# Performance work log

Measured on AMD Instinct MI355X. Metric: run time of the kernel, lower is better.

## Reference

```python
import jax, jax.numpy as jnp
import numpy as np

NUM_HEADS = 8

def setup_inputs() -> dict:
    key = jax.random.key(0)
    ks = jax.random.split(key, 7)
    B, Cin, H, W = 4, 256, 56, 56
    Cout = 256
    s = 1.0 / np.sqrt(Cin)
    return {
        "x": jax.random.normal(ks[0], (B, Cin, H, W), dtype=jnp.float32),
        "wq": jax.random.normal(ks[1], (Cout, Cin), dtype=jnp.float32) * s,
        "bq": jax.random.normal(ks[2], (Cout,), dtype=jnp.float32) * s,
        "wk": jax.random.normal(ks[3], (Cout, Cin), dtype=jnp.float32) * s,
        "bk": jax.random.normal(ks[4], (Cout,), dtype=jnp.float32) * s,
        "wv": jax.random.normal(ks[5], (Cout, Cin), dtype=jnp.float32) * s,
        "bv": jax.random.normal(ks[6], (Cout,), dtype=jnp.float32) * s,
    }

def _proj(x, w, b):
    # 1x1 conv == per-pixel linear: [B,Cin,H,W] x [Cout,Cin] -> [B,Cout,H,W]
    return jnp.einsum('bchw,oc->bohw', x, w) + b[None, :, None, None]

def reference(x, wq, bq, wk, bk, wv, bv):
    B, _, H, W = x.shape
    Cout = wq.shape[0]
    hd = Cout // NUM_HEADS
    N = H * W
    # project and reshape to [B, heads, N, head_dim]
    def split_heads(t):
        return t.reshape(B, NUM_HEADS, hd, N).transpose(0, 1, 3, 2)
    q = split_heads(_proj(x, wq, bq))
    k = split_heads(_proj(x, wk, bk))
    v = split_heads(_proj(x, wv, bv))
    scores = jnp.einsum('bhnd,bhmd->bhnm', q, k) / jnp.sqrt(jnp.float32(hd))
    attn = jax.nn.softmax(scores, axis=-1)          # [B, heads, N, N]
    out = jnp.einsum('bhnm,bhmd->bhnd', attn, v)    # [B, heads, N, hd]
    out = out.transpose(0, 1, 3, 2).reshape(B, Cout, H, W)
    return out
```

## Files before the change

### kernel.cpp

```cpp
#include <hip/hip_runtime.h>
#include <math.h>


#define NB   4
#define CIN  256
#define NPIX 3136
#define NH   8
#define HD   32
#define QSC  0.25503837897544295f

typedef float          f32x4  __attribute__((ext_vector_type(4)));
typedef short          bf16x8 __attribute__((ext_vector_type(8)));
typedef unsigned int   u32x4  __attribute__((ext_vector_type(4)));
typedef unsigned int   u32x2  __attribute__((ext_vector_type(2)));
typedef unsigned short u16x4  __attribute__((ext_vector_type(4)));

static __device__ __forceinline__ unsigned short f2bf(float f) {
  union { float f; unsigned u; } v; v.f = f;
  return (unsigned short)((v.u + 0x7fffu + ((v.u >> 16) & 1u)) >> 16);
}

static __device__ __forceinline__ float fast_exp2(float x) {
  float r;
  asm("v_exp_f32 %0, %1" : "=v"(r) : "v"(x));
  return r;
}

static __device__ __forceinline__ unsigned cvt_pk_bf16(float lo, float hi) {
  unsigned r;
  asm("v_cvt_pk_bf16_f32 %0, %1, %2" : "=v"(r) : "v"(lo), "v"(hi));
  return r;
}

static __device__ __forceinline__ void gload_lds16(const void* g, void* l) {
  __builtin_amdgcn_global_load_lds(
      (__attribute__((address_space(1))) const void*)g,
      (__attribute__((address_space(3))) void*)l, 16, 0, 0);
}

static __device__ __forceinline__ bf16x8 lds_frag16(const unsigned char* p) {
  u32x4 u = *(const u32x4*)p;
  return __builtin_bit_cast(bf16x8, u);
}

__global__ __launch_bounds__(256) void k_xpose(const float* __restrict__ x,
                                               unsigned short* __restrict__ xbT) {
  __shared__ unsigned short tile[64][66];
  const int n0 = blockIdx.x * 64, c0 = blockIdx.y * 64, b = blockIdx.z;
  const int t = threadIdx.x;
  const int cl = t >> 4, nl = (t & 15) * 4;
#pragma unroll
  for (int rep = 0; rep < 4; ++rep) {
    const int c = cl + rep * 16;
    f32x4 v = *(const f32x4*)(x + ((size_t)(b * CIN + c0 + c)) * NPIX + n0 + nl);
    tile[nl + 0][c] = f2bf(v.x);
    tile[nl + 1][c] = f2bf(v.y);
    tile[nl + 2][c] = f2bf(v.z);
    tile[nl + 3][c] = f2bf(v.w);
  }
  __syncthreads();
  const int nr = t >> 2, co = (t & 3) * 16;
  unsigned pw[8];
#pragma unroll
  for (int j = 0; j < 8; ++j)
    pw[j] = (unsigned)tile[nr][co + 2 * j] | ((unsigned)tile[nr][co + 2 * j + 1] << 16);
  unsigned short* dst = xbT + ((size_t)(b * NPIX + n0 + nr)) * 256 + c0 + co;
  u32x4 lo = {pw[0], pw[1], pw[2], pw[3]};
  u32x4 hi = {pw[4], pw[5], pw[6], pw[7]};
  *(u32x4*)dst = lo;
  *(u32x4*)(dst + 8) = hi;
}

__global__ __launch_bounds__(256) void k_wconv(const float* __restrict__ wq,
                                               const float* __restrict__ wk,
                                               const float* __restrict__ wv,
                                               unsigned short* __restrict__ wb) {
  const int i = blockIdx.x * 256 + threadIdx.x;
  const int mat = i >> 16, idx = i & 65535;
  const float* w = (mat == 0) ? wq : (mat == 1 ? wk : wv);
  const float s = (mat == 0) ? QSC : 1.0f;
  wb[i] = f2bf(w[idx] * s);
}

__global__ __launch_bounds__(256) void k_proj(
    const unsigned short* __restrict__ xbT, const unsigned short* __restrict__ wb,
    const float* __restrict__ bq, const float* __restrict__ bk,
    const float* __restrict__ bv,
    unsigned short* __restrict__ qws, unsigned short* __restrict__ kws,
    unsigned short* __restrict__ vtws) {
  __shared__ alignas(16) unsigned char lds[20480];
  const int b = blockIdx.y & 3, mat = blockIdx.y >> 2;
  const int n0 = blockIdx.x * 64;
  const int t = threadIdx.x, l = t & 63, wid = t >> 6, g = l >> 4, q = l & 15;
  const unsigned short* wmat = wb + mat * (256 * 256);

  f32x4 acc[4][4] = {};

  for (int ks = 0; ks < 8; ++ks) {
#pragma unroll
    for (int r = 0; r < 4; ++r) {
      const unsigned short* src = wmat + ((wid + 4 * r) * 16 + q) * 256 + ks * 32 + g * 8;
      gload_lds16(src, lds + (r * 256 + t) * 16);
    }
    gload_lds16(xbT + ((size_t)(b * NPIX + n0 + wid * 16 + q)) * 256 + ks * 32 + g * 8,
                lds + 16384 + t * 16);
    __syncthreads();

    bf16x8 wa[4], xf[4];
#pragma unroll
    for (int r = 0; r < 4; ++r) wa[r] = lds_frag16(lds + (r * 256 + wid * 64 + l) * 16);
#pragma unroll
    for (int nt = 0; nt < 4; ++nt) xf[nt] = lds_frag16(lds + 16384 + (nt * 64 + l) * 16);
#pragma unroll
    for (int r = 0; r < 4; ++r)
#pragma unroll
      for (int nt = 0; nt < 4; ++nt)
        acc[r][nt] = __builtin_amdgcn_mfma_f32_16x16x32_bf16(wa[r], xf[nt], acc[r][nt], 0, 0, 0);
    __syncthreads();
  }

  const float* bias = (mat == 0) ? bq : (mat == 1 ? bk : bv);
  const float bsc = (mat == 0) ? QSC : 1.0f;
#pragma unroll
  for (int r = 0; r < 4; ++r) {
    const int ob = (wid + 4 * r) * 16 + g * 4;
    const int h = ob >> 5, d0 = ob & 31;
    const float b0 = bias[ob + 0] * bsc, b1 = bias[ob + 1] * bsc;
    const float b2 = bias[ob + 2] * bsc, b3 = bias[ob + 3] * bsc;
#pragma unroll
    for (int nt = 0; nt < 4; ++nt) {
      const int n = n0 + nt * 16 + q;
      f32x4 a = acc[r][nt];
      if (mat < 2) {
        unsigned short* dst = (mat == 0) ? qws : kws;
        u16x4 pk = {f2bf(a.x + b0), f2bf(a.y + b1), f2bf(a.z + b2), f2bf(a.w + b3)};
        *(u16x4*)(dst + ((size_t)((b * NH + h) * NPIX + n)) * HD + d0) = pk;
      } else {
        unsigned short* vr = vtws + ((size_t)((b * NH + h) * HD + d0)) * NPIX + n;
        vr[0] = f2bf(a.x + b0);
        vr[(size_t)NPIX] = f2bf(a.y + b1);
        vr[(size_t)2 * NPIX] = f2bf(a.z + b2);
        vr[(size_t)3 * NPIX] = f2bf(a.w + b3);
      }
    }
  }
}

__global__ __launch_bounds__(256) void k_attn(
    const unsigned short* __restrict__ qws, const unsigned short* __restrict__ kws,
    const unsigned short* __restrict__ vtws, float* __restrict__ out) {
  __shared__ alignas(16) unsigned char lds[32768];
  const int bid = blockIdx.x;
  const int xcd = bid & 7, inner = bid >> 3;
  const int qt = inner % 25;
  const int bh = 8 * (inner / 25) + xcd;
  const int q0 = qt * 128;
  const int t = threadIdx.x, l = t & 63, wid = t >> 6, g = l >> 4, q = l & 15;

  const int nA = q0 + wid * 32 + q;
  const int nB = nA + 16;
  const int rowA = (nA < NPIX) ? nA : (NPIX - 1);
  const int rowB = (nB < NPIX) ? nB : (NPIX - 1);

  u32x4 quA = *(const u32x4*)(qws + ((size_t)(bh * NPIX + rowA)) * HD + g * 8);
  u32x4 quB = *(const u32x4*)(qws + ((size_t)(bh * NPIX + rowB)) * HD + g * 8);
  const bf16x8 qfA = __builtin_bit_cast(bf16x8, quA);
  const bf16x8 qfB = __builtin_bit_cast(bf16x8, quB);
  const u32x4 onesu = {0x3F803F80u, 0x3F803F80u, 0x3F803F80u, 0x3F803F80u};
  const bf16x8 onesf = __builtin_bit_cast(bf16x8, onesu);
  const f32x4 zero4 = {0.f, 0.f, 0.f, 0.f};

  f32x4 oA0 = zero4, oA1 = zero4, oB0 = zero4, oB1 = zero4;
  f32x4 sumA = zero4, sumB = zero4;

  const unsigned short* ksrc = kws + ((size_t)(bh * NPIX + wid * 16 + q)) * HD + g * 8;
  const unsigned short* vsrc =
      vtws + ((size_t)(bh * HD + (wid >> 1) * 16 + q)) * NPIX + (wid & 1) * 32 + g * 8;

  unsigned char* const pbaseA = lds + 16384 + wid * 4096;
  unsigned char* const pbaseB = pbaseA + 2048;

  unsigned bofs = 0;
  gload_lds16(ksrc, lds + t * 16);
  gload_lds16(vsrc, lds + 4096 + t * 16);
  __syncthreads();

  for (int kt = 0; kt < 49; ++kt) {
    if (kt < 48) {
      gload_lds16(ksrc + (size_t)(kt + 1) * 64 * HD, lds + (bofs ^ 8192) + t * 16);
      gload_lds16(vsrc + (kt + 1) * 64, lds + (bofs ^ 8192) + 4096 + t * 16);
    }
    const unsigned char* kb = lds + bofs;
    const unsigned char* vb = lds + bofs + 4096;

    f32x4 sA[4], sB[4];
    __builtin_amdgcn_s_setprio(1);
#pragma unroll
    for (int jj = 0; jj < 4; ++jj) {
      bf16x8 kf = lds_frag16(kb + (jj * 64 + l) * 16);
      sA[jj] = __builtin_amdgcn_mfma_f32_16x16x32_bf16(kf, qfA, zero4, 0, 0, 0);
      sB[jj] = __builtin_amdgcn_mfma_f32_16x16x32_bf16(kf, qfB, zero4, 0, 0, 0);
    }
    __builtin_amdgcn_s_setprio(0);

    {
      unsigned pw[8];
#pragma unroll
      for (int jj = 0; jj < 4; ++jj) {
#pragma unroll
        for (int rp = 0; rp < 2; ++rp) {
          float p0 = fast_exp2(sA[jj][2 * rp + 0]);
          float p1 = fast_exp2(sA[jj][2 * rp + 1]);
          pw[jj * 2 + rp] = cvt_pk_bf16(p0, p1);
        }
      }
      u32x4 c0 = {pw[0], pw[1], pw[2], pw[3]};
      u32x4 c1 = {pw[4], pw[5], pw[6], pw[7]};
      *(u32x4*)(pbaseA + l * 16) = c0;
      *(u32x4*)(pbaseA + 1024 + l * 16) = c1;
    }
    {
      unsigned pw[8];
#pragma unroll
      for (int jj = 0; jj < 4; ++jj) {
#pragma unroll
        for (int rp = 0; rp < 2; ++rp) {
          float p0 = fast_exp2(sB[jj][2 * rp + 0]);
          float p1 = fast_exp2(sB[jj][2 * rp + 1]);
          pw[jj * 2 + rp] = cvt_pk_bf16(p0, p1);
        }
      }
      u32x4 c0 = {pw[0], pw[1], pw[2], pw[3]};
      u32x4 c1 = {pw[4], pw[5], pw[6], pw[7]};
      *(u32x4*)(pbaseB + l * 16) = c0;
      *(u32x4*)(pbaseB + 1024 + l * 16) = c1;
    }

    asm volatile("s_waitcnt lgkmcnt(0)" ::: "memory");
    __builtin_amdgcn_sched_barrier(0);

#pragma unroll
    for (int c = 0; c < 2; ++c) {
      bf16x8 v0 = lds_frag16(vb + (c * 64 + l) * 16);
      bf16x8 v1 = lds_frag16(vb + (128 + c * 64 + l) * 16);

      const unsigned char* pA = pbaseA + c * 1024 + q * 16 + (g & 2) * 4;
      u32x2 alo = *(const u32x2*)(pA + ((2 * g) & 3) * 256);
      u32x2 ahi = *(const u32x2*)(pA + ((2 * g + 1) & 3) * 256);
      u32x4 au = {alo.x, alo.y, ahi.x, ahi.y};
      bf16x8 pfA = __builtin_bit_cast(bf16x8, au);

      const unsigned char* pB = pbaseB + c * 1024 + q * 16 + (g & 2) * 4;
      u32x2 blo = *(const u32x2*)(pB + ((2 * g) & 3) * 256);
      u32x2 bhi = *(const u32x2*)(pB + ((2 * g + 1) & 3) * 256);
      u32x4 bu = {blo.x, blo.y, bhi.x, bhi.y};
      bf16x8 pfB = __builtin_bit_cast(bf16x8, bu);

      __builtin_amdgcn_s_setprio(1);
      oA0 = __builtin_amdgcn_mfma_f32_16x16x32_bf16(v0, pfA, oA0, 0, 0, 0);
      oA1 = __builtin_amdgcn_mfma_f32_16x16x32_bf16(v1, pfA, oA1, 0, 0, 0);
      sumA = __builtin_amdgcn_mfma_f32_16x16x32_bf16(onesf, pfA, sumA, 0, 0, 0);
      oB0 = __builtin_amdgcn_mfma_f32_16x16x32_bf16(v0, pfB, oB0, 0, 0, 0);
      oB1 = __builtin_amdgcn_mfma_f32_16x16x32_bf16(v1, pfB, oB1, 0, 0, 0);
      sumB = __builtin_amdgcn_mfma_f32_16x16x32_bf16(onesf, pfB, sumB, 0, 0, 0);
      __builtin_amdgcn_s_setprio(0);
    }

    __syncthreads();
    bofs ^= 8192;
  }

  if (nA < NPIX) {
    const float inv = 1.0f / sumA[0];
    float* ob = out + (size_t)(bh * HD) * NPIX + nA;
#pragma unroll
    for (int r = 0; r < 4; ++r) {
      ob[(size_t)(g * 4 + r) * NPIX] = oA0[r] * inv;
      ob[(size_t)(16 + g * 4 + r) * NPIX] = oA1[r] * inv;
    }
  }
  if (nB < NPIX) {
    const float inv = 1.0f / sumB[0];
    float* ob = out + (size_t)(bh * HD) * NPIX + nB;
#pragma unroll
    for (int r = 0; r < 4; ++r) {
      ob[(size_t)(g * 4 + r) * NPIX] = oB0[r] * inv;
      ob[(size_t)(16 + g * 4 + r) * NPIX] = oB1[r] * inv;
    }
  }
}

extern "C" void kernel_launch(void* const* d_in, const int* in_sizes, int n_in,
                              void* d_out, int out_size, void* d_ws, size_t ws_size,
                              hipStream_t stream) {
  const float* x  = (const float*)d_in[0];
  const float* wq = (const float*)d_in[1];
  const float* bq = (const float*)d_in[2];
  const float* wk = (const float*)d_in[3];
  const float* bk = (const float*)d_in[4];
  const float* wv = (const float*)d_in[5];
  const float* bv = (const float*)d_in[6];
  float* out = (float*)d_out;

  unsigned char* ws = (unsigned char*)d_ws;
  unsigned short* xbT  = (unsigned short*)(ws);
  unsigned short* wb   = (unsigned short*)(ws + 6422528);
  unsigned short* qws  = (unsigned short*)(ws + 6815744);
  unsigned short* kws  = (unsigned short*)(ws + 13238272);
  unsigned short* vtws = (unsigned short*)(ws + 19660800);

  k_xpose<<<dim3(49, 4, 4), 256, 0, stream>>>(x, xbT);
  k_wconv<<<dim3(768), 256, 0, stream>>>(wq, wk, wv, wb);
  k_proj<<<dim3(49, 12), 256, 0, stream>>>(xbT, wb, bq, bk, bv, qws, kws, vtws);
  k_attn<<<dim3(800), 256, 0, stream>>>(qws, kws, vtws, out);
}
```

Baseline: 115.4 us.

## Give each wave a private K/V tile copy to drop block-wide barriers

Each of the four waves now loads the whole 64-key K and V tile into its own LDS region instead of sharing one double-buffered tile. The per-iteration __syncthreads is replaced by wave-local vmcnt/lgkmcnt waits. The aim is to remove cross-wave barrier stalls and let waves drift independently. In exchange, global-to-LDS traffic is four times higher, LDS use grows to 48KB, and double buffering is lost: the next tile is only issued after compute finishes and then waited on immediately, which exposes load latency.

```diff
diff --git a/kernel.cpp b/kernel.cpp
--- a/kernel.cpp
+++ b/kernel.cpp
@@ -149,7 +149,7 @@
 __global__ __launch_bounds__(256) void k_attn(
     const unsigned short* __restrict__ qws, const unsigned short* __restrict__ kws,
     const unsigned short* __restrict__ vtws, float* __restrict__ out) {
-  __shared__ alignas(16) unsigned char lds[32768];
+  __shared__ alignas(16) unsigned char lds[49152];
   const int bid = blockIdx.x;
   const int xcd = bid & 7, inner = bid >> 3;
   const int qt = inner % 25;
@@ -173,25 +173,35 @@
   f32x4 oA0 = zero4, oA1 = zero4, oB0 = zero4, oB1 = zero4;
   f32x4 sumA = zero4, sumB = zero4;
 
-  const unsigned short* ksrc = kws + ((size_t)(bh * NPIX + wid * 16 + q)) * HD + g * 8;
-  const unsigned short* vsrc =
-      vtws + ((size_t)(bh * HD + (wid >> 1) * 16 + q)) * NPIX + (wid & 1) * 32 + g * 8;
-
-  unsigned char* const pbaseA = lds + 16384 + wid * 4096;
+  unsigned char* const kvb = lds + wid * 8192;
+  unsigned char* const pbaseA = lds + 32768 + wid * 4096;
   unsigned char* const pbaseB = pbaseA + 2048;
 
-  unsigned bofs = 0;
-  gload_lds16(ksrc, lds + t * 16);
-  gload_lds16(vsrc, lds + 4096 + t * 16);
-  __syncthreads();
+  const unsigned short* kp[4];
+  const unsigned short* vp[4];
+#pragma unroll
+  for (int ss = 0; ss < 4; ++ss) {
+    kp[ss] = kws + ((size_t)(bh * NPIX + ss * 16 + q)) * HD + g * 8;
+    vp[ss] = vtws + ((size_t)(bh * HD + (ss >> 1) * 16 + q)) * NPIX + (ss & 1) * 32 + g * 8;
+  }
+
+#define STG(kt_)                                                             \
+  do {                                                                       \
+    _Pragma("unroll")                                                        \
+    for (int ss = 0; ss < 4; ++ss) {                                         \
+      gload_lds16(kp[ss] + (size_t)(kt_) * 64 * HD, kvb + ss * 1024 + l * 16); \
+      gload_lds16(vp[ss] + (size_t)(kt_) * 64, kvb + 4096 + ss * 1024 + l * 16); \
+    }                                                                        \
+  } while (0)
+
+  STG(0);
 
   for (int kt = 0; kt < 49; ++kt) {
-    if (kt < 48) {
-      gload_lds16(ksrc + (size_t)(kt + 1) * 64 * HD, lds + (bofs ^ 8192) + t * 16);
-      gload_lds16(vsrc + (kt + 1) * 64, lds + (bofs ^ 8192) + 4096 + t * 16);
-    }
-    const unsigned char* kb = lds + bofs;
-    const unsigned char* vb = lds + bofs + 4096;
+    asm volatile("s_waitcnt vmcnt(0)" ::: "memory");
+    __builtin_amdgcn_sched_barrier(0);
+
+    const unsigned char* kb = kvb;
+    const unsigned char* vb = kvb + 4096;
 
     f32x4 sA[4], sB[4];
     __builtin_amdgcn_s_setprio(1);
@@ -266,9 +276,12 @@
       __builtin_amdgcn_s_setprio(0);
     }
 
-    __syncthreads();
-    bofs ^= 8192;
-  }
+    asm volatile("s_waitcnt lgkmcnt(0)" ::: "memory");
+    __builtin_amdgcn_sched_barrier(0);
+
+    if (kt < 48) STG(kt + 1);
+  }
+#undef STG
 
   if (nA < NPIX) {
     const float inv = 1.0f / sumA[0];
```

Measured after the change: 179.2 us. 55.3% more time.

## Load K/V tiles directly into registers, dropping shared LDS staging and block barriers

Applied to the files above, without the earlier changes.

Each wave now loads its own K and V^T fragments straight from global memory into registers, with a register double buffer prefetching the next tile. The cooperative LDS staging, the K/V LDS buffers and the per-iteration __syncthreads are removed, which halves LDS use and lets waves run independently. In exchange each wave re-reads the whole K/V tile from global memory/L2 (4x redundant traffic per block), and register pressure rises from holding the prefetched fragments.

```diff
diff --git a/kernel.cpp b/kernel.cpp
--- a/kernel.cpp
+++ b/kernel.cpp
@@ -149,7 +149,7 @@
 __global__ __launch_bounds__(256) void k_attn(
     const unsigned short* __restrict__ qws, const unsigned short* __restrict__ kws,
     const unsigned short* __restrict__ vtws, float* __restrict__ out) {
-  __shared__ alignas(16) unsigned char lds[32768];
+  __shared__ alignas(16) unsigned char lds[16384];
   const int bid = blockIdx.x;
   const int xcd = bid & 7, inner = bid >> 3;
   const int qt = inner % 25;
@@ -173,31 +173,41 @@
   f32x4 oA0 = zero4, oA1 = zero4, oB0 = zero4, oB1 = zero4;
   f32x4 sumA = zero4, sumB = zero4;
 
-  const unsigned short* ksrc = kws + ((size_t)(bh * NPIX + wid * 16 + q)) * HD + g * 8;
-  const unsigned short* vsrc =
-      vtws + ((size_t)(bh * HD + (wid >> 1) * 16 + q)) * NPIX + (wid & 1) * 32 + g * 8;
-
-  unsigned char* const pbaseA = lds + 16384 + wid * 4096;
+  const unsigned short* kbase = kws + ((size_t)(bh * NPIX + q)) * HD + g * 8;
+  const unsigned short* vbase = vtws + ((size_t)(bh * HD + q)) * NPIX + g * 8;
+
+  unsigned char* const pbaseA = lds + wid * 4096;
   unsigned char* const pbaseB = pbaseA + 2048;
 
-  unsigned bofs = 0;
-  gload_lds16(ksrc, lds + t * 16);
-  gload_lds16(vsrc, lds + 4096 + t * 16);
-  __syncthreads();
+  u32x4 kcur[4], vcur[2][2], knxt[4], vnxt[2][2];
+#pragma unroll
+  for (int jj = 0; jj < 4; ++jj)
+    kcur[jj] = *(const u32x4*)(kbase + (size_t)(jj * 16) * HD);
+#pragma unroll
+  for (int h = 0; h < 2; ++h)
+#pragma unroll
+    for (int c = 0; c < 2; ++c)
+      vcur[h][c] = *(const u32x4*)(vbase + (size_t)(h * 16) * NPIX + c * 32);
 
   for (int kt = 0; kt < 49; ++kt) {
     if (kt < 48) {
-      gload_lds16(ksrc + (size_t)(kt + 1) * 64 * HD, lds + (bofs ^ 8192) + t * 16);
-      gload_lds16(vsrc + (kt + 1) * 64, lds + (bofs ^ 8192) + 4096 + t * 16);
-    }
-    const unsigned char* kb = lds + bofs;
-    const unsigned char* vb = lds + bofs + 4096;
+      const size_t ko = (size_t)((kt + 1) * 64) * HD;
+      const int vo = (kt + 1) * 64;
+#pragma unroll
+      for (int jj = 0; jj < 4; ++jj)
+        knxt[jj] = *(const u32x4*)(kbase + ko + (size_t)(jj * 16) * HD);
+#pragma unroll
+      for (int h = 0; h < 2; ++h)
+#pragma unroll
+        for (int c = 0; c < 2; ++c)
+          vnxt[h][c] = *(const u32x4*)(vbase + (size_t)(h * 16) * NPIX + vo + c * 32);
+    }
 
     f32x4 sA[4], sB[4];
     __builtin_amdgcn_s_setprio(1);
 #pragma unroll
     for (int jj = 0; jj < 4; ++jj) {
-      bf16x8 kf = lds_frag16(kb + (jj * 64 + l) * 16);
+      bf16x8 kf = __builtin_bit_cast(bf16x8, kcur[jj]);
       sA[jj] = __builtin_amdgcn_mfma_f32_16x16x32_bf16(kf, qfA, zero4, 0, 0, 0);
       sB[jj] = __builtin_amdgcn_mfma_f32_16x16x32_bf16(kf, qfB, zero4, 0, 0, 0);
     }
@@ -241,8 +251,8 @@
 
 #pragma unroll
     for (int c = 0; c < 2; ++c) {
-      bf16x8 v0 = lds_frag16(vb + (c * 64 + l) * 16);
-      bf16x8 v1 = lds_frag16(vb + (128 + c * 64 + l) * 16);
+      bf16x8 v0 = __builtin_bit_cast(bf16x8, vcur[0][c]);
+      bf16x8 v1 = __builtin_bit_cast(bf16x8, vcur[1][c]);
 
       const unsigned char* pA = pbaseA + c * 1024 + q * 16 + (g & 2) * 4;
       u32x2 alo = *(const u32x2*)(pA + ((2 * g) & 3) * 256);
@@ -266,8 +276,14 @@
       __builtin_amdgcn_s_setprio(0);
     }
 
-    __syncthreads();
-    bofs ^= 8192;
+#pragma unroll
+    for (int jj = 0; jj < 4; ++jj) kcur[jj] = knxt[jj];
+#pragma unroll
+    for (int h = 0; h < 2; ++h)
+#pragma unroll
+      for (int c = 0; c < 2; ++c) vcur[h][c] = vnxt[h][c];
+
+    __builtin_amdgcn_sched_barrier(0);
   }
 
   if (nA < NPIX) {
```

New measurement: 166.8 us. 44.5% more time.
